# Performance work log

Hardware: AMD Instinct MI355X
Metric: run time of the kernel (lower is better)

## Reference

```python
import jax, jax.numpy as jnp
import numpy as np

B, L, F, P = 128, 256, 4, 4   # dialogs, dialog length, future/past links
IN, H, C = 1024, 256, 7
N = B * L


def _build_edges():
    # same structure as build_intra_graph: self-loop + F future + P past per node
    i = np.arange(L)
    ss, tt = [], []
    for d in range(-P, F + 1):
        j = i + d
        m = (j >= 0) & (j < L)
        ss.append(i[m]); tt.append(j[m])
    s = np.concatenate(ss); t = np.concatenate(tt)
    offs = (np.arange(B) * L)[:, None]
    S = (s[None, :] + offs).ravel()
    T = (t[None, :] + offs).ravel()
    return np.stack([S, T]).astype(np.int32)


def setup_inputs() -> dict:
    key = jax.random.key(0)
    ks = jax.random.split(key, 16)
    ei = _build_edges()
    speakers = np.asarray(jax.random.randint(ks[0], (N,), 0, 2), dtype=np.int32)
    rel = (speakers[ei[0]] * speakers[ei[1]]).astype(np.int32)
    sd_in = 1.0 / np.sqrt(IN)
    sd_h = 1.0 / np.sqrt(H)
    return {
        "input": jax.random.normal(ks[1], (N, IN), jnp.float32),
        "dialog_lengths": jnp.full((B,), L, jnp.int32),
        "speakers": jnp.asarray(speakers),
        "labels": jax.random.randint(ks[2], (N,), 0, C, jnp.int32),
        "edge_index": jnp.asarray(ei),
        "rel_type": jnp.asarray(rel),
        # RGCNConv(IN, H, num_relations=2): per-relation weight, root weight, bias
        "W_rgcn": jax.random.normal(ks[3], (2, IN, H), jnp.float32) * sd_in,
        "W_root": jax.random.normal(ks[4], (IN, H), jnp.float32) * sd_in,
        "b_rgcn": jax.random.normal(ks[5], (H,), jnp.float32) * 0.01,
        # GraphConv(H, H): lin_rel (on aggregated neighbors, with bias), lin_root (no bias)
        "W_rel": jax.random.normal(ks[6], (H, H), jnp.float32) * sd_h,
        "b_rel": jax.random.normal(ks[7], (H,), jnp.float32) * 0.01,
        "W_grt": jax.random.normal(ks[8], (H, H), jnp.float32) * sd_h,
        # skip_con: Linear(IN, H)
        "W_skip": jax.random.normal(ks[9], (IN, H), jnp.float32) * sd_in,
        "b_skip": jax.random.normal(ks[10], (H,), jnp.float32) * 0.01,
        # classify: Linear(H, C)
        "W_cls": jax.random.normal(ks[11], (H, C), jnp.float32) * sd_h,
        "b_cls": jax.random.normal(ks[12], (C,), jnp.float32) * 0.01,
    }


def reference(input, dialog_lengths, speakers, labels, edge_index, rel_type,
              W_rgcn, W_root, b_rgcn, W_rel, b_rel, W_grt,
              W_skip, b_skip, W_cls, b_cls):
    n = input.shape[0]
    src, dst = edge_index[0], edge_index[1]
    seg = jax.ops.segment_sum

    # --- RGCNConv: out_i = x_i @ W_root + b + sum_r mean_{j in N_r(i)} x_j @ W_r
    t = jnp.einsum('ni,rio->rno', input, W_rgcn)      # [2, N, H]
    msg = t[rel_type, src]                            # [E, H] relation-specific messages
    h = input @ W_root + b_rgcn
    for r in range(2):
        m = (rel_type == r).astype(input.dtype)       # [E]
        s = seg(msg * m[:, None], dst, num_segments=n)
        cnt = seg(m, dst, num_segments=n)
        h = h + s / jnp.maximum(cnt, 1.0)[:, None]    # mean aggregation per relation

    # --- GraphConv (aggr='add'): out_i = W_rel @ sum_j h_j + b_rel + W_grt @ h_i
    neigh = seg(h[src], dst, num_segments=n)          # [N, H]
    h2 = neigh @ W_rel + b_rel + h @ W_grt

    # --- skip connection + classifier
    out = (h2 + input @ W_skip + b_skip) @ W_cls + b_cls  # [N, C]

    # --- cross entropy (mean)
    logp = jax.nn.log_softmax(out, axis=-1)
    loss = -jnp.mean(jnp.take_along_axis(logp, labels[:, None].astype(jnp.int32), axis=1))
    return out, loss
```

## Files before the change

kernel.cpp:

```cpp
#include <hip/hip_runtime.h>

#define NN 32768
#define INF 1024
#define HF 256

typedef __bf16 bf16x8 __attribute__((ext_vector_type(8)));
typedef float f32x4 __attribute__((ext_vector_type(4)));
typedef unsigned short u16x8 __attribute__((ext_vector_type(8)));

__device__ __forceinline__ float bf2f(unsigned short u) {
  union { unsigned int i; float f; } v; v.i = ((unsigned int)u) << 16; return v.f;
}
__device__ __forceinline__ unsigned short f2bf(float f) {
  union { float f; unsigned int i; } v; v.f = f;
  unsigned int x = v.i;
  return (unsigned short)((x + 0x7fffu + ((x >> 16) & 1u)) >> 16);
}

__device__ __forceinline__ void ld_lds16(const unsigned short* g, unsigned short* l) {
  __builtin_amdgcn_global_load_lds(
      (__attribute__((address_space(1))) const unsigned int*)g,
      (__attribute__((address_space(3))) unsigned int*)l, 16, 0, 0);
}

__global__ __launch_bounds__(256)
void diagcn_prep(const float* __restrict__ x, const float* __restrict__ Wrgcn,
                 const float* __restrict__ Wroot, const float* __restrict__ Wskip,
                 const float* __restrict__ Wgrt, const float* __restrict__ Wrel,
                 unsigned short* __restrict__ Xbf, unsigned short* __restrict__ WbigT,
                 unsigned short* __restrict__ WsmT, float* __restrict__ loss) {
  int bid = blockIdx.x;
  if (bid < 32768) {
    if (bid == 0 && threadIdx.x == 0) loss[0] = 0.f;
    int idx = bid * 256 + threadIdx.x;
    float4 v = ((const float4*)x)[idx];
    ushort4 u; u.x = f2bf(v.x); u.y = f2bf(v.y); u.z = f2bf(v.z); u.w = f2bf(v.w);
    ((ushort4*)Xbf)[idx] = u;
    return;
  }
  __shared__ float tile[64 * 65];
  int tb = bid - 32768;
  const float* src;
  int k0, ncol0;
  unsigned short* dst;
  int ldd, nrow0;
  if (tb < 256) {
    int tn = tb >> 4, tk = tb & 15;
    int mat = tn >> 2;
    src = (mat == 0) ? Wrgcn : (mat == 1) ? (Wrgcn + 262144) : (mat == 2) ? Wroot : Wskip;
    k0 = tk * 64; ncol0 = (tn & 3) * 64;
    dst = WbigT; ldd = 1024; nrow0 = tn * 64;
  } else {
    int t2 = tb - 256;
    int tn = t2 >> 3, tk = t2 & 7;
    src = (tk < 4) ? Wgrt : Wrel;
    k0 = (tk & 3) * 64; ncol0 = tn * 64;
    dst = WsmT; ldd = 512; nrow0 = tn * 64;
  }
  int kdst0 = (tb < 256) ? k0 : (((tb - 256) & 7) * 64);
  int c = threadIdx.x & 63, rb = threadIdx.x >> 6;
#pragma unroll
  for (int it = 0; it < 16; ++it) {
    int r = rb + it * 4;
    tile[r * 65 + c] = src[(size_t)(k0 + r) * 256 + ncol0 + c];
  }
  __syncthreads();
  int kk = threadIdx.x & 63;
#pragma unroll
  for (int it = 0; it < 16; ++it) {
    int nn = rb + it * 4;
    dst[(size_t)(nrow0 + nn) * ldd + kdst0 + kk] = f2bf(tile[kk * 65 + nn]);
  }
}

template<bool STG>
__device__ __forceinline__ void g1_tile(int t,
    const unsigned short* __restrict__ gA0, const unsigned short* __restrict__ gB0,
    unsigned short* SH, int w, int abase, int bbase, int sw8,
    f32x4 (&acc)[8][4]) {
  unsigned short* Ab = SH + ((t & 3) << 14);
  unsigned short* Bb = Ab + 8192;
  bf16x8 av[4], bv[4];
#pragma unroll
  for (int i = 0; i < 4; ++i)
    av[i] = *(const bf16x8*)&Ab[(abase + i * 16) * 32 + sw8];
#pragma unroll
  for (int j = 0; j < 4; ++j)
    bv[j] = *(const bf16x8*)&Bb[(bbase + j * 16) * 32 + sw8];
  if (STG) {
    unsigned short* d = SH + (((t + 3) & 3) << 14) + (w << 10);
    const unsigned short* g = gA0 + (t + 3) * 32;
    ld_lds16(g, d);
    ld_lds16(g + 16 * 1024, d + 512);
  }
  __builtin_amdgcn_s_barrier();
  asm volatile("s_waitcnt lgkmcnt(0)");
  __builtin_amdgcn_s_setprio(1);
#pragma unroll
  for (int i = 0; i < 4; ++i)
#pragma unroll
    for (int j = 0; j < 4; ++j)
      acc[i][j] = __builtin_amdgcn_mfma_f32_16x16x32_bf16(av[i], bv[j], acc[i][j], 0, 0, 0);
  __builtin_amdgcn_s_setprio(0);
  __builtin_amdgcn_s_barrier();
#pragma unroll
  for (int i = 0; i < 4; ++i)
    av[i] = *(const bf16x8*)&Ab[(abase + 64 + i * 16) * 32 + sw8];
  if (STG) {
    unsigned short* d = SH + (((t + 3) & 3) << 14) + 8192 + (w << 10);
    const unsigned short* g = gB0 + (t + 3) * 32;
    ld_lds16(g, d);
    ld_lds16(g + 16 * 1024, d + 512);
  }
  __builtin_amdgcn_s_barrier();
  asm volatile("s_waitcnt lgkmcnt(0)");
  __builtin_amdgcn_s_setprio(1);
#pragma unroll
  for (int i = 0; i < 4; ++i)
#pragma unroll
    for (int j = 0; j < 4; ++j)
      acc[4 + i][j] = __builtin_amdgcn_mfma_f32_16x16x32_bf16(av[i], bv[j], acc[4 + i][j], 0, 0, 0);
  __builtin_amdgcn_s_setprio(0);
}

__global__ __launch_bounds__(512, 2)
void diagcn_gemm1(const unsigned short* __restrict__ A, const unsigned short* __restrict__ BT,
                  unsigned short* __restrict__ Y) {
  __shared__ unsigned short SH[65536];
  const int tid = threadIdx.x;
  const int w = tid >> 6, lane = tid & 63;
  const int quad = lane >> 4, l15 = lane & 15;
  const int wm = w >> 2, wn = w & 3;
  const int b = blockIdx.x;
  const int wg = ((b & 7) << 6) + (b >> 3);
  const int m0 = (wg >> 2) << 8;
  const int n0 = (wg & 3) << 8;
  const int abase = wm * 128 + l15;
  const int bbase = wn * 64 + l15;
  const int sw8 = ((quad ^ ((l15 >> 1) & 3)) << 3);
  const int csrc8 = (((lane & 3) ^ ((lane >> 3) & 3)) << 3);
  const unsigned short* gA0 = A + (size_t)(m0 + w * 32 + (lane >> 2)) * 1024 + csrc8;
  const unsigned short* gB0 = BT + (size_t)(n0 + w * 32 + (lane >> 2)) * 1024 + csrc8;

  f32x4 acc[8][4] = {};

#pragma unroll
  for (int tt = 0; tt < 3; ++tt) {
    unsigned short* dA = SH + (tt << 14) + (w << 10);
    ld_lds16(gA0 + tt * 32, dA);
    ld_lds16(gA0 + tt * 32 + 16 * 1024, dA + 512);
    unsigned short* dB = SH + (tt << 14) + 8192 + (w << 10);
    ld_lds16(gB0 + tt * 32, dB);
    ld_lds16(gB0 + tt * 32 + 16 * 1024, dB + 512);
  }
  asm volatile("s_waitcnt vmcnt(8)" ::: "memory");
  __builtin_amdgcn_s_barrier();

#pragma unroll 1
  for (int t = 0; t < 29; ++t) {
    g1_tile<true>(t, gA0, gB0, SH, w, abase, bbase, sw8, acc);
    asm volatile("s_waitcnt vmcnt(8)" ::: "memory");
    __builtin_amdgcn_s_barrier();
  }
  g1_tile<false>(29, gA0, gB0, SH, w, abase, bbase, sw8, acc);
  asm volatile("s_waitcnt vmcnt(4)" ::: "memory");
  __builtin_amdgcn_s_barrier();
  g1_tile<false>(30, gA0, gB0, SH, w, abase, bbase, sw8, acc);
  asm volatile("s_waitcnt vmcnt(0)" ::: "memory");
  __builtin_amdgcn_s_barrier();
  g1_tile<false>(31, gA0, gB0, SH, w, abase, bbase, sw8, acc);

#pragma unroll
  for (int i = 0; i < 8; ++i)
#pragma unroll
    for (int j = 0; j < 4; ++j) {
      const int row = m0 + wm * 128 + i * 16 + quad * 4;
      const int col = n0 + wn * 64 + j * 16 + l15;
#pragma unroll
      for (int r = 0; r < 4; ++r)
        Y[(size_t)(row + r) * 1024 + col] = f2bf(acc[i][j][r]);
    }
}

__global__ __launch_bounds__(256)
void diagcn_h(const unsigned short* __restrict__ Y, const int* __restrict__ spk,
              const float* __restrict__ brgcn, unsigned short* __restrict__ A2) {
  int b = blockIdx.x;
  int wv = threadIdx.x >> 6, lane = threadIdx.x & 63;
  int half = lane >> 5, li = lane & 31, c0 = li << 3;
  int node = ((b & 7) << 12) + ((b >> 3) << 3) + wv * 2 + half;
  int p = node & 255, dbase = node - p;
  int si = spk[node];
  float a0[8] = {}, a1[8] = {};
  float n0 = 0.f, n1 = 0.f;
#pragma unroll
  for (int d = -4; d <= 4; ++d) {
    int pj = p + d;
    float w = (pj >= 0 && pj < 256) ? 1.f : 0.f;
    int jc = pj < 0 ? 0 : (pj > 255 ? 255 : pj);
    int nj = dbase + jc;
    int rel = si & spk[nj];
    u16x8 v = *(const u16x8*)&Y[(size_t)nj * 1024 + (rel << 8) + c0];
    float w1 = rel ? w : 0.f, w0 = rel ? 0.f : w;
#pragma unroll
    for (int k = 0; k < 8; ++k) {
      float f = bf2f(v[k]);
      a0[k] += f * w0; a1[k] += f * w1;
    }
    n0 += w0; n1 += w1;
  }
  u16x8 vr = *(const u16x8*)&Y[(size_t)node * 1024 + 512 + c0];
  float i0 = 1.f / fmaxf(n0, 1.f), i1 = 1.f / fmaxf(n1, 1.f);
  u16x8 u;
#pragma unroll
  for (int k = 0; k < 8; ++k)
    u[k] = f2bf(bf2f(vr[k]) + brgcn[c0 + k] + a0[k] * i0 + a1[k] * i1);
  *(u16x8*)&A2[(size_t)node * 512 + c0] = u;
}

__global__ __launch_bounds__(256)
void diagcn_neigh(unsigned short* __restrict__ A2) {
  int b = blockIdx.x;
  int wv = threadIdx.x >> 6, lane = threadIdx.x & 63;
  int half = lane >> 5, li = lane & 31, c0 = li << 3;
  int node = ((b & 7) << 12) + ((b >> 3) << 3) + wv * 2 + half;
  int p = node & 255, dbase = node - p;
  float s[8] = {};
#pragma unroll
  for (int d = -4; d <= 4; ++d) {
    int pj = p + d;
    float w = (pj >= 0 && pj < 256) ? 1.f : 0.f;
    int jc = pj < 0 ? 0 : (pj > 255 ? 255 : pj);
    u16x8 v = *(const u16x8*)&A2[(size_t)(dbase + jc) * 512 + c0];
#pragma unroll
    for (int k = 0; k < 8; ++k) s[k] += bf2f(v[k]) * w;
  }
  u16x8 u;
#pragma unroll
  for (int k = 0; k < 8; ++k) u[k] = f2bf(s[k]);
  *(u16x8*)&A2[(size_t)node * 512 + 256 + c0] = u;
}

__global__ __launch_bounds__(256)
void diagcn_gemm2(const unsigned short* __restrict__ A, const unsigned short* __restrict__ BT,
                  const unsigned short* __restrict__ Y, const float* __restrict__ Wcls,
                  const float* __restrict__ bcls, const float* __restrict__ brel,
                  const float* __restrict__ bskip, const int* __restrict__ labels,
                  float* __restrict__ out, float* __restrict__ loss) {
  const int K = 512;
  __shared__ unsigned short As[64 * 64];
  __shared__ unsigned short Bs[256 * 64];
  __shared__ float Wc[2312];
  for (int i = threadIdx.x; i < 2312; i += 256) {
    float v;
    if (i < 1792) v = Wcls[i];
    else if (i < 1799) v = bcls[i - 1792];
    else if (i < 1800) v = 0.f;
    else if (i < 2056) v = brel[i - 1800];
    else v = bskip[i - 2056];
    Wc[i] = v;
  }
  const int tid = threadIdx.x;
  const int w = tid >> 6, lane = tid & 63;
  const int quad = lane >> 4, l15 = lane & 15;
  const int b = blockIdx.x;
  const int m0 = (((b & 7) << 6) + (b >> 3)) << 6;
  const int rowg = lane >> 3;
  const int kbsw = (lane & 7) ^ rowg;

  f32x4 acc[16] = {};
  const unsigned short* Abase = A + (size_t)m0 * K + kbsw * 8;
  const unsigned short* Bbase = BT + kbsw * 8;

  for (int k0 = 0; k0 < K; k0 += 64) {
#pragma unroll
    for (int t = 0; t < 2; ++t) {
      int grp = w * 2 + t;
      ld_lds16(Abase + (size_t)(grp * 8 + rowg) * K + k0, &As[grp * 512]);
    }
#pragma unroll
    for (int t = 0; t < 8; ++t) {
      int grp = w * 8 + t;
      ld_lds16(Bbase + (size_t)(grp * 8 + rowg) * K + k0, &Bs[grp * 512]);
    }
    __syncthreads();
#pragma unroll
    for (int ks = 0; ks < 2; ++ks) {
      int kb = ks * 4 + quad;
      int ra = w * 16 + l15;
      bf16x8 av = *(const bf16x8*)&As[ra * 64 + ((kb ^ (ra & 7)) << 3)];
#pragma unroll
      for (int j = 0; j < 16; ++j) {
        int rb2 = j * 16 + l15;
        bf16x8 bv = *(const bf16x8*)&Bs[rb2 * 64 + ((kb ^ (rb2 & 7)) << 3)];
        acc[j] = __builtin_amdgcn_mfma_f32_16x16x32_bf16(av, bv, acc[j], 0, 0, 0);
      }
    }
    __syncthreads();
  }

  float wsum[4][7] = {};
#pragma unroll
  for (int j = 0; j < 16; ++j) {
    int col = j * 16 + l15;
    float bb = Wc[1800 + col] + Wc[2056 + col];
#pragma unroll
    for (int r = 0; r < 4; ++r) {
      int row = m0 + w * 16 + quad * 4 + r;
      float z = acc[j][r] + bb + bf2f(Y[(size_t)row * 1024 + 768 + col]);
#pragma unroll
      for (int c = 0; c < 7; ++c) wsum[r][c] += z * Wc[col * 7 + c];
    }
  }
#pragma unroll
  for (int o = 1; o < 16; o <<= 1)
#pragma unroll
    for (int r = 0; r < 4; ++r)
#pragma unroll
      for (int c = 0; c < 7; ++c) wsum[r][c] += __shfl_xor(wsum[r][c], o, 64);

  float lsum = 0.f;
#pragma unroll
  for (int r = 0; r < 4; ++r) {
    int row = m0 + w * 16 + quad * 4 + r;
    float o7[7], mx = -1e30f;
#pragma unroll
    for (int c = 0; c < 7; ++c) {
      o7[c] = wsum[r][c] + Wc[1792 + c];
      mx = fmaxf(mx, o7[c]);
    }
    if (l15 < 7) out[(size_t)row * 7 + l15] = o7[l15];
    float s = 0.f;
#pragma unroll
    for (int c = 0; c < 7; ++c) s += expf(o7[c] - mx);
    int lab = labels[row];
    lsum += mx + logf(s) - o7[lab];
  }
  lsum += __shfl_xor(lsum, 16, 64);
  lsum += __shfl_xor(lsum, 32, 64);
  if (lane == 0) atomicAdd(loss, lsum * (1.0f / (float)NN));
}

extern "C" void kernel_launch(void* const* d_in, const int* in_sizes, int n_in,
                              void* d_out, int out_size, void* d_ws, size_t ws_size,
                              hipStream_t stream) {
  const float* x      = (const float*)d_in[0];
  const int* speakers = (const int*)d_in[2];
  const int* labels   = (const int*)d_in[3];
  const float* Wrgcn  = (const float*)d_in[6];
  const float* Wroot  = (const float*)d_in[7];
  const float* brgcn  = (const float*)d_in[8];
  const float* Wrel   = (const float*)d_in[9];
  const float* brel   = (const float*)d_in[10];
  const float* Wgrt   = (const float*)d_in[11];
  const float* Wskip  = (const float*)d_in[12];
  const float* bskip  = (const float*)d_in[13];
  const float* Wcls   = (const float*)d_in[14];
  const float* bcls   = (const float*)d_in[15];
  float* out = (float*)d_out;
  float* loss = out + (size_t)NN * 7;

  const size_t OFF_XBF  = 0;
  const size_t OFF_WBIG = 67108864;
  const size_t OFF_WSM  = 69206016;
  const size_t OFF_Y    = 69468160;
  const size_t OFF_A2   = 136577024;
  const size_t NEED     = 170131456;
  if (ws_size < NEED) return;

  char* ws = (char*)d_ws;
  unsigned short* Xbf   = (unsigned short*)(ws + OFF_XBF);
  unsigned short* WbigT = (unsigned short*)(ws + OFF_WBIG);
  unsigned short* WsmT  = (unsigned short*)(ws + OFF_WSM);
  unsigned short* Y     = (unsigned short*)(ws + OFF_Y);
  unsigned short* A2    = (unsigned short*)(ws + OFF_A2);

  diagcn_prep<<<dim3(33056), dim3(256), 0, stream>>>(x, Wrgcn, Wroot, Wskip, Wgrt, Wrel,
                                                     Xbf, WbigT, WsmT, loss);
  diagcn_gemm1<<<dim3(512), dim3(512), 0, stream>>>(Xbf, WbigT, Y);
  diagcn_h<<<dim3(NN / 8), dim3(256), 0, stream>>>(Y, speakers, brgcn, A2);
  diagcn_neigh<<<dim3(NN / 8), dim3(256), 0, stream>>>(A2);
  diagcn_gemm2<<<dim3(512), dim3(256), 0, stream>>>(A2, WsmT, Y, Wcls, bcls, brel, bskip,
                                                    labels, out, loss);
}
```

Before: 372.2 us.

## Software-pipeline LDS fragment loads across K tiles in GEMM1 main loop

Restructures the GEMM1 K-loop so the A/B register fragments for the next tile are read from LDS while the current tile's MFMAs run. Double-buffered register sets alternate between iterations, and the loop is unrolled by two. Barriers drop from four to two per tile, and partial lgkmcnt waits replace full drains. This is meant to hide LDS read latency and barrier stalls behind matrix math, at the cost of more VGPRs, which could cause spills at two workgroups per CU.

```diff
diff --git a/kernel.cpp b/kernel.cpp
--- a/kernel.cpp
+++ b/kernel.cpp
@@ -73,28 +73,31 @@
   }
 }
 
-template<bool STG>
+template<bool STG, int VM, bool LAST>
 __device__ __forceinline__ void g1_tile(int t,
     const unsigned short* __restrict__ gA0, const unsigned short* __restrict__ gB0,
     unsigned short* SH, int w, int abase, int bbase, int sw8,
+    bf16x8 (&av)[4], bf16x8 (&bv)[4], bf16x8 (&nav)[4], bf16x8 (&nbv)[4],
     f32x4 (&acc)[8][4]) {
   unsigned short* Ab = SH + ((t & 3) << 14);
   unsigned short* Bb = Ab + 8192;
-  bf16x8 av[4], bv[4];
+  bf16x8 av2[4];
 #pragma unroll
   for (int i = 0; i < 4; ++i)
-    av[i] = *(const bf16x8*)&Ab[(abase + i * 16) * 32 + sw8];
-#pragma unroll
-  for (int j = 0; j < 4; ++j)
-    bv[j] = *(const bf16x8*)&Bb[(bbase + j * 16) * 32 + sw8];
+    av2[i] = *(const bf16x8*)&Ab[(abase + 64 + i * 16) * 32 + sw8];
+  __builtin_amdgcn_sched_barrier(0);
   if (STG) {
-    unsigned short* d = SH + (((t + 3) & 3) << 14) + (w << 10);
-    const unsigned short* g = gA0 + (t + 3) * 32;
-    ld_lds16(g, d);
-    ld_lds16(g + 16 * 1024, d + 512);
-  }
-  __builtin_amdgcn_s_barrier();
-  asm volatile("s_waitcnt lgkmcnt(0)");
+    unsigned short* dA = SH + (((t + 3) & 3) << 14) + (w << 10);
+    const unsigned short* gA = gA0 + (t + 3) * 32;
+    ld_lds16(gA, dA);
+    ld_lds16(gA + 16 * 1024, dA + 512);
+    unsigned short* dB = SH + (((t + 3) & 3) << 14) + 8192 + (w << 10);
+    const unsigned short* gB = gB0 + (t + 3) * 32;
+    ld_lds16(gB, dB);
+    ld_lds16(gB + 16 * 1024, dB + 512);
+  }
+  asm volatile("s_waitcnt lgkmcnt(4)");
+  __builtin_amdgcn_sched_barrier(0);
   __builtin_amdgcn_s_setprio(1);
 #pragma unroll
   for (int i = 0; i < 4; ++i)
@@ -102,25 +105,49 @@
     for (int j = 0; j < 4; ++j)
       acc[i][j] = __builtin_amdgcn_mfma_f32_16x16x32_bf16(av[i], bv[j], acc[i][j], 0, 0, 0);
   __builtin_amdgcn_s_setprio(0);
+  __builtin_amdgcn_sched_barrier(0);
+  if constexpr (VM == 8) asm volatile("s_waitcnt vmcnt(8)" ::: "memory");
+  else if constexpr (VM == 4) asm volatile("s_waitcnt vmcnt(4)" ::: "memory");
+  else if constexpr (VM == 0) asm volatile("s_waitcnt vmcnt(0)" ::: "memory");
   __builtin_amdgcn_s_barrier();
-#pragma unroll
-  for (int i = 0; i < 4; ++i)
-    av[i] = *(const bf16x8*)&Ab[(abase + 64 + i * 16) * 32 + sw8];
-  if (STG) {
-    unsigned short* d = SH + (((t + 3) & 3) << 14) + 8192 + (w << 10);
-    const unsigned short* g = gB0 + (t + 3) * 32;
-    ld_lds16(g, d);
-    ld_lds16(g + 16 * 1024, d + 512);
-  }
-  __builtin_amdgcn_s_barrier();
-  asm volatile("s_waitcnt lgkmcnt(0)");
-  __builtin_amdgcn_s_setprio(1);
-#pragma unroll
-  for (int i = 0; i < 4; ++i)
+  if constexpr (!LAST) {
+    unsigned short* An = SH + (((t + 1) & 3) << 14);
+    unsigned short* Bn = An + 8192;
+#pragma unroll
+    for (int i = 0; i < 4; ++i)
+      nav[i] = *(const bf16x8*)&An[(abase + i * 16) * 32 + sw8];
+    __builtin_amdgcn_sched_barrier(0);
+    asm volatile("s_waitcnt lgkmcnt(4)");
+    __builtin_amdgcn_sched_barrier(0);
+    __builtin_amdgcn_s_setprio(1);
+#pragma unroll
+    for (int i = 0; i < 2; ++i)
+#pragma unroll
+      for (int j = 0; j < 4; ++j)
+        acc[4 + i][j] = __builtin_amdgcn_mfma_f32_16x16x32_bf16(av2[i], bv[j], acc[4 + i][j], 0, 0, 0);
+    __builtin_amdgcn_s_setprio(0);
+    __builtin_amdgcn_sched_barrier(0);
 #pragma unroll
     for (int j = 0; j < 4; ++j)
-      acc[4 + i][j] = __builtin_amdgcn_mfma_f32_16x16x32_bf16(av[i], bv[j], acc[4 + i][j], 0, 0, 0);
-  __builtin_amdgcn_s_setprio(0);
+      nbv[j] = *(const bf16x8*)&Bn[(bbase + j * 16) * 32 + sw8];
+    __builtin_amdgcn_sched_barrier(0);
+    __builtin_amdgcn_s_setprio(1);
+#pragma unroll
+    for (int i = 2; i < 4; ++i)
+#pragma unroll
+      for (int j = 0; j < 4; ++j)
+        acc[4 + i][j] = __builtin_amdgcn_mfma_f32_16x16x32_bf16(av2[i], bv[j], acc[4 + i][j], 0, 0, 0);
+    __builtin_amdgcn_s_setprio(0);
+    __builtin_amdgcn_s_barrier();
+  } else {
+    asm volatile("s_waitcnt lgkmcnt(0)");
+    __builtin_amdgcn_sched_barrier(0);
+#pragma unroll
+    for (int i = 0; i < 4; ++i)
+#pragma unroll
+      for (int j = 0; j < 4; ++j)
+        acc[4 + i][j] = __builtin_amdgcn_mfma_f32_16x16x32_bf16(av2[i], bv[j], acc[4 + i][j], 0, 0, 0);
+  }
 }
 
 __global__ __launch_bounds__(512, 2)
@@ -143,6 +170,7 @@
   const unsigned short* gB0 = BT + (size_t)(n0 + w * 32 + (lane >> 2)) * 1024 + csrc8;
 
   f32x4 acc[8][4] = {};
+  bf16x8 avA[4], bvA[4], avB[4], bvB[4];
 
 #pragma unroll
   for (int tt = 0; tt < 3; ++tt) {
@@ -155,20 +183,25 @@
   }
   asm volatile("s_waitcnt vmcnt(8)" ::: "memory");
   __builtin_amdgcn_s_barrier();
+#pragma unroll
+  for (int i = 0; i < 4; ++i)
+    avA[i] = *(const bf16x8*)&SH[(abase + i * 16) * 32 + sw8];
+#pragma unroll
+  for (int j = 0; j < 4; ++j)
+    bvA[j] = *(const bf16x8*)&SH[8192 + (bbase + j * 16) * 32 + sw8];
+  __builtin_amdgcn_sched_barrier(0);
 
 #pragma unroll 1
-  for (int t = 0; t < 29; ++t) {
-    g1_tile<true>(t, gA0, gB0, SH, w, abase, bbase, sw8, acc);
-    asm volatile("s_waitcnt vmcnt(8)" ::: "memory");
-    __builtin_amdgcn_s_barrier();
-  }
-  g1_tile<false>(29, gA0, gB0, SH, w, abase, bbase, sw8, acc);
-  asm volatile("s_waitcnt vmcnt(4)" ::: "memory");
-  __builtin_amdgcn_s_barrier();
-  g1_tile<false>(30, gA0, gB0, SH, w, abase, bbase, sw8, acc);
-  asm volatile("s_waitcnt vmcnt(0)" ::: "memory");
-  __builtin_amdgcn_s_barrier();
-  g1_tile<false>(31, gA0, gB0, SH, w, abase, bbase, sw8, acc);
+  for (int tt = 0; tt < 14; ++tt) {
+    g1_tile<true, 8, false>(2 * tt, gA0, gB0, SH, w, abase, bbase, sw8,
+                            avA, bvA, avB, bvB, acc);
+    g1_tile<true, 8, false>(2 * tt + 1, gA0, gB0, SH, w, abase, bbase, sw8,
+                            avB, bvB, avA, bvA, acc);
+  }
+  g1_tile<true, 8, false>(28, gA0, gB0, SH, w, abase, bbase, sw8, avA, bvA, avB, bvB, acc);
+  g1_tile<false, 4, false>(29, gA0, gB0, SH, w, abase, bbase, sw8, avB, bvB, avA, bvA, acc);
+  g1_tile<false, 0, false>(30, gA0, gB0, SH, w, abase, bbase, sw8, avA, bvA, avB, bvB, acc);
+  g1_tile<false, -1, true>(31, gA0, gB0, SH, w, abase, bbase, sw8, avB, bvB, avA, bvA, acc);
 
 #pragma unroll
   for (int i = 0; i < 8; ++i)
```

Measured after the change: 366.6 us. About the same (-1.5%).

## Restructure GEMM1 mainloop to K=64 double-buffered tiles with staggered A/B prefetch

Applied to the files above, without the earlier changes.

Rewrites the bf16 GEMM main loop from a four-stage K=32 ring buffer to two K=64 buffers. A and B prefetches are split and staggered across four MFMA sub-phases, with a new swizzled LDS layout and fewer barriers per unit of K. Occupancy hint drops from 2 to 1 block per CU, since 128KB of LDS per block no longer allows two. The aim is fewer loop iterations and sync points plus larger MFMA bursts, at the cost of less latency hiding through occupancy and more complex hazard ordering.

```diff
diff --git a/kernel.cpp b/kernel.cpp
--- a/kernel.cpp
+++ b/kernel.cpp
@@ -21,6 +21,10 @@
   __builtin_amdgcn_global_load_lds(
       (__attribute__((address_space(1))) const unsigned int*)g,
       (__attribute__((address_space(3))) unsigned int*)l, 16, 0, 0);
+}
+
+__device__ __forceinline__ f32x4 MF(bf16x8 a, bf16x8 b, f32x4 c) {
+  return __builtin_amdgcn_mfma_f32_16x16x32_bf16(a, b, c, 0, 0, 0);
 }
 
 __global__ __launch_bounds__(256)
@@ -73,57 +77,108 @@
   }
 }
 
-template<bool STG>
+template<int BUF, bool STGA, bool STGB, int VM>
 __device__ __forceinline__ void g1_tile(int t,
-    const unsigned short* __restrict__ gA0, const unsigned short* __restrict__ gB0,
-    unsigned short* SH, int w, int abase, int bbase, int sw8,
+    const unsigned short* __restrict__ gA, const unsigned short* __restrict__ gB,
+    unsigned short* SH, int w, int aoff0, int aoff1, int boff0, int boff1,
     f32x4 (&acc)[8][4]) {
-  unsigned short* Ab = SH + ((t & 3) << 14);
-  unsigned short* Bb = Ab + 8192;
-  bf16x8 av[4], bv[4];
-#pragma unroll
-  for (int i = 0; i < 4; ++i)
-    av[i] = *(const bf16x8*)&Ab[(abase + i * 16) * 32 + sw8];
-#pragma unroll
-  for (int j = 0; j < 4; ++j)
-    bv[j] = *(const bf16x8*)&Bb[(bbase + j * 16) * 32 + sw8];
-  if (STG) {
-    unsigned short* d = SH + (((t + 3) & 3) << 14) + (w << 10);
-    const unsigned short* g = gA0 + (t + 3) * 32;
-    ld_lds16(g, d);
-    ld_lds16(g + 16 * 1024, d + 512);
-  }
+  const unsigned short* Rb = SH + BUF * 32768;
+  bf16x8 av[8], bv[8];
+#pragma unroll
+  for (int mi = 0; mi < 4; ++mi) {
+    av[mi * 2 + 0] = *(const bf16x8*)&Rb[aoff0 + mi * 1024];
+    av[mi * 2 + 1] = *(const bf16x8*)&Rb[aoff1 + mi * 1024];
+  }
+#pragma unroll
+  for (int nj = 0; nj < 2; ++nj) {
+    bv[nj * 2 + 0] = *(const bf16x8*)&Rb[boff0 + nj * 1024];
+    bv[nj * 2 + 1] = *(const bf16x8*)&Rb[boff1 + nj * 1024];
+  }
+  if (STGA) {
+    const unsigned short* g = gA + (size_t)(t + 1) * 64;
+    unsigned short* d = SH + (BUF ^ 1) * 32768 + w * 512;
+    ld_lds16(g, d); ld_lds16(g + 65536, d + 4096);
+  }
+  asm volatile("s_waitcnt lgkmcnt(8)");
   __builtin_amdgcn_s_barrier();
   asm volatile("s_waitcnt lgkmcnt(0)");
+  __builtin_amdgcn_sched_barrier(0);
   __builtin_amdgcn_s_setprio(1);
 #pragma unroll
-  for (int i = 0; i < 4; ++i)
-#pragma unroll
-    for (int j = 0; j < 4; ++j)
-      acc[i][j] = __builtin_amdgcn_mfma_f32_16x16x32_bf16(av[i], bv[j], acc[i][j], 0, 0, 0);
+  for (int mi = 0; mi < 4; ++mi)
+#pragma unroll
+    for (int nj = 0; nj < 2; ++nj) {
+      acc[mi][nj] = MF(av[mi * 2 + 0], bv[nj * 2 + 0], acc[mi][nj]);
+      acc[mi][nj] = MF(av[mi * 2 + 1], bv[nj * 2 + 1], acc[mi][nj]);
+    }
   __builtin_amdgcn_s_setprio(0);
   __builtin_amdgcn_s_barrier();
 #pragma unroll
-  for (int i = 0; i < 4; ++i)
-    av[i] = *(const bf16x8*)&Ab[(abase + 64 + i * 16) * 32 + sw8];
-  if (STG) {
-    unsigned short* d = SH + (((t + 3) & 3) << 14) + 8192 + (w << 10);
-    const unsigned short* g = gB0 + (t + 3) * 32;
-    ld_lds16(g, d);
-    ld_lds16(g + 16 * 1024, d + 512);
+  for (int nj = 2; nj < 4; ++nj) {
+    bv[nj * 2 + 0] = *(const bf16x8*)&Rb[boff0 + nj * 1024];
+    bv[nj * 2 + 1] = *(const bf16x8*)&Rb[boff1 + nj * 1024];
+  }
+  if (STGA) {
+    const unsigned short* g = gA + (size_t)(t + 1) * 64 + 131072;
+    unsigned short* d = SH + (BUF ^ 1) * 32768 + 8192 + w * 512;
+    ld_lds16(g, d); ld_lds16(g + 65536, d + 4096);
   }
   __builtin_amdgcn_s_barrier();
   asm volatile("s_waitcnt lgkmcnt(0)");
+  __builtin_amdgcn_sched_barrier(0);
   __builtin_amdgcn_s_setprio(1);
 #pragma unroll
-  for (int i = 0; i < 4; ++i)
-#pragma unroll
-    for (int j = 0; j < 4; ++j)
-      acc[4 + i][j] = __builtin_amdgcn_mfma_f32_16x16x32_bf16(av[i], bv[j], acc[4 + i][j], 0, 0, 0);
+  for (int mi = 0; mi < 4; ++mi)
+#pragma unroll
+    for (int nj = 2; nj < 4; ++nj) {
+      acc[mi][nj] = MF(av[mi * 2 + 0], bv[nj * 2 + 0], acc[mi][nj]);
+      acc[mi][nj] = MF(av[mi * 2 + 1], bv[nj * 2 + 1], acc[mi][nj]);
+    }
   __builtin_amdgcn_s_setprio(0);
-}
-
-__global__ __launch_bounds__(512, 2)
+  __builtin_amdgcn_s_barrier();
+#pragma unroll
+  for (int mi = 0; mi < 4; ++mi) {
+    av[mi * 2 + 0] = *(const bf16x8*)&Rb[aoff0 + 4096 + mi * 1024];
+    av[mi * 2 + 1] = *(const bf16x8*)&Rb[aoff1 + 4096 + mi * 1024];
+  }
+  if (STGB) {
+    const unsigned short* g = gB + (size_t)(t + 2) * 64;
+    unsigned short* d = SH + BUF * 32768 + 16384 + w * 512;
+    ld_lds16(g, d); ld_lds16(g + 65536, d + 4096);
+  }
+  __builtin_amdgcn_s_barrier();
+  asm volatile("s_waitcnt lgkmcnt(0)");
+  __builtin_amdgcn_sched_barrier(0);
+  __builtin_amdgcn_s_setprio(1);
+#pragma unroll
+  for (int mi = 0; mi < 4; ++mi)
+#pragma unroll
+    for (int nj = 0; nj < 2; ++nj) {
+      acc[4 + mi][nj] = MF(av[mi * 2 + 0], bv[nj * 2 + 0], acc[4 + mi][nj]);
+      acc[4 + mi][nj] = MF(av[mi * 2 + 1], bv[nj * 2 + 1], acc[4 + mi][nj]);
+    }
+  __builtin_amdgcn_s_setprio(0);
+  __builtin_amdgcn_s_barrier();
+  if (STGB) {
+    const unsigned short* g = gB + (size_t)(t + 2) * 64 + 131072;
+    unsigned short* d = SH + BUF * 32768 + 24576 + w * 512;
+    ld_lds16(g, d); ld_lds16(g + 65536, d + 4096);
+  }
+  __builtin_amdgcn_s_setprio(1);
+#pragma unroll
+  for (int mi = 0; mi < 4; ++mi)
+#pragma unroll
+    for (int nj = 2; nj < 4; ++nj) {
+      acc[4 + mi][nj] = MF(av[mi * 2 + 0], bv[nj * 2 + 0], acc[4 + mi][nj]);
+      acc[4 + mi][nj] = MF(av[mi * 2 + 1], bv[nj * 2 + 1], acc[4 + mi][nj]);
+    }
+  __builtin_amdgcn_s_setprio(0);
+  if constexpr (VM == 4) asm volatile("s_waitcnt vmcnt(4)" ::: "memory");
+  else if constexpr (VM == 0) asm volatile("s_waitcnt vmcnt(0)" ::: "memory");
+  if constexpr (VM >= 0) __builtin_amdgcn_s_barrier();
+}
+
+__global__ __launch_bounds__(512, 1)
 void diagcn_gemm1(const unsigned short* __restrict__ A, const unsigned short* __restrict__ BT,
                   unsigned short* __restrict__ Y) {
   __shared__ unsigned short SH[65536];
@@ -135,40 +190,38 @@
   const int wg = ((b & 7) << 6) + (b >> 3);
   const int m0 = (wg >> 2) << 8;
   const int n0 = (wg & 3) << 8;
-  const int abase = wm * 128 + l15;
-  const int bbase = wn * 64 + l15;
-  const int sw8 = ((quad ^ ((l15 >> 1) & 3)) << 3);
-  const int csrc8 = (((lane & 3) ^ ((lane >> 3) & 3)) << 3);
-  const unsigned short* gA0 = A + (size_t)(m0 + w * 32 + (lane >> 2)) * 1024 + csrc8;
-  const unsigned short* gB0 = BT + (size_t)(n0 + w * 32 + (lane >> 2)) * 1024 + csrc8;
+  const int c0 = ((quad ^ (l15 & 7)) << 3);
+  const int c1 = (((4 + quad) ^ (l15 & 7)) << 3);
+  const int aoff0 = wm * 8192 + l15 * 64 + c0;
+  const int aoff1 = wm * 8192 + l15 * 64 + c1;
+  const int boff0 = 16384 + (wn >> 1) * 8192 + ((wn & 1) * 64 + l15) * 64 + c0;
+  const int boff1 = 16384 + (wn >> 1) * 8192 + ((wn & 1) * 64 + l15) * 64 + c1;
+  const int ln3 = lane >> 3;
+  const int csrc = ((lane & 7) ^ ln3) << 3;
+  const unsigned short* gA = A + (size_t)(m0 + w * 8 + ln3) * 1024 + csrc;
+  const unsigned short* gB = BT + (size_t)(n0 + w * 8 + ln3) * 1024 + csrc;
 
   f32x4 acc[8][4] = {};
 
-#pragma unroll
-  for (int tt = 0; tt < 3; ++tt) {
-    unsigned short* dA = SH + (tt << 14) + (w << 10);
-    ld_lds16(gA0 + tt * 32, dA);
-    ld_lds16(gA0 + tt * 32 + 16 * 1024, dA + 512);
-    unsigned short* dB = SH + (tt << 14) + 8192 + (w << 10);
-    ld_lds16(gB0 + tt * 32, dB);
-    ld_lds16(gB0 + tt * 32 + 16 * 1024, dB + 512);
-  }
-  asm volatile("s_waitcnt vmcnt(8)" ::: "memory");
+  {
+    unsigned short* d;
+    d = SH + w * 512;                 ld_lds16(gA, d);                    ld_lds16(gA + 65536, d + 4096);
+    d = SH + 8192 + w * 512;          ld_lds16(gA + 131072, d);           ld_lds16(gA + 131072 + 65536, d + 4096);
+    d = SH + 16384 + w * 512;         ld_lds16(gB, d);                    ld_lds16(gB + 65536, d + 4096);
+    d = SH + 24576 + w * 512;         ld_lds16(gB + 131072, d);           ld_lds16(gB + 131072 + 65536, d + 4096);
+    d = SH + 32768 + 16384 + w * 512; ld_lds16(gB + 64, d);               ld_lds16(gB + 64 + 65536, d + 4096);
+    d = SH + 32768 + 24576 + w * 512; ld_lds16(gB + 64 + 131072, d);      ld_lds16(gB + 64 + 131072 + 65536, d + 4096);
+  }
+  asm volatile("s_waitcnt vmcnt(4)" ::: "memory");
   __builtin_amdgcn_s_barrier();
 
 #pragma unroll 1
-  for (int t = 0; t < 29; ++t) {
-    g1_tile<true>(t, gA0, gB0, SH, w, abase, bbase, sw8, acc);
-    asm volatile("s_waitcnt vmcnt(8)" ::: "memory");
-    __builtin_amdgcn_s_barrier();
-  }
-  g1_tile<false>(29, gA0, gB0, SH, w, abase, bbase, sw8, acc);
-  asm volatile("s_waitcnt vmcnt(4)" ::: "memory");
-  __builtin_amdgcn_s_barrier();
-  g1_tile<false>(30, gA0, gB0, SH, w, abase, bbase, sw8, acc);
-  asm volatile("s_waitcnt vmcnt(0)" ::: "memory");
-  __builtin_amdgcn_s_barrier();
-  g1_tile<false>(31, gA0, gB0, SH, w, abase, bbase, sw8, acc);
+  for (int u = 0; u < 7; ++u) {
+    g1_tile<0, true, true, 4>(2 * u,     gA, gB, SH, w, aoff0, aoff1, boff0, boff1, acc);
+    g1_tile<1, true, true, 4>(2 * u + 1, gA, gB, SH, w, aoff0, aoff1, boff0, boff1, acc);
+  }
+  g1_tile<0, true,  false, 0>(14, gA, gB, SH, w, aoff0, aoff1, boff0, boff1, acc);
+  g1_tile<1, false, false, -1>(15, gA, gB, SH, w, aoff0, aoff1, boff0, boff1, acc);
 
 #pragma unroll
   for (int i = 0; i < 8; ++i)
```

Measured after the change: 368.0 us. No clear change (-1.1%).
